# Performance work log

Hardware: AMD Instinct MI355X
Metric: run time of the kernel (lower is better)

## Reference

```python
import jax, jax.numpy as jnp
import numpy as np

# --- constants from the source module's globals ---
TAU_M, TAU_S = 8.0, 2.0
EM = float(np.exp(-1.0 / TAU_M))   # exp(-1/tau_m)
ES = float(np.exp(-1.0 / TAU_S))   # exp(-1/tau_s)
ETA = TAU_M / (TAU_M - TAU_S)
# dual-exponential PSP kernel eta*(e^{-t/tau_m}-e^{-t/tau_s}) as a 2nd-order IIR
A1_0 = EM + ES          # y[t-1] coefficient
A2_0 = -(EM * ES)       # y[t-2] coefficient
B_0 = ETA * (EM - ES)   # x[t] coefficient
THRESH, RESET_DECAY, RESET_V = 1.0, EM, 1.0
BATCH, T, IN = 64, 300, 300


def spike_fn(v):
    return (v >= THRESH).astype(v.dtype)


def dual_exp_iir(x, a1, a2, b):
    """Per-feature 2nd-order IIR over time. x: [B, F, T] -> [B, F, T]."""
    xt = jnp.moveaxis(x, -1, 0)  # [T, B, F]

    def step(carry, xc):
        y1, y2 = carry
        y = a1 * y1 + a2 * y2 + b * xc
        return (y, y1), y

    z = jnp.zeros_like(xt[0])
    _, ys = jax.lax.scan(step, (z, z), xt)
    return jnp.moveaxis(ys, 0, -1)


def lif_dense(x, W, bias):
    """Dense synapse + spiking neuron with decaying reset (membrane_filter=False).
    x: [B, Fin, T] -> spikes [B, Fout, T]."""
    # time-independent linear map: batch all T GEMMs into one einsum
    cur = jnp.einsum('bit,oi->bot', x, W) + bias[None, :, None]
    ct = jnp.moveaxis(cur, -1, 0)  # [T, B, Fout]

    def step(reset, c):
        v = c + reset                       # no membrane integration (membrane_filter=False)
        s = spike_fn(v)
        reset = reset * RESET_DECAY - s * RESET_V  # decaying post-spike reset
        return reset, s

    _, spikes = jax.lax.scan(step, jnp.zeros_like(ct[0]), ct)
    return jnp.moveaxis(spikes, 0, -1)


def setup_inputs() -> dict:
    key = jax.random.key(0)
    ks = jax.random.split(key, 8)
    inputs = (jax.random.uniform(ks[0], (BATCH, IN, T)) < 0.2).astype(jnp.float32)

    def coeffs(f):
        return (jnp.full((f,), A1_0, jnp.float32),
                jnp.full((f,), A2_0, jnp.float32),
                jnp.full((f,), B_0, jnp.float32))

    def dense(k, fin, fout):
        w = (jax.random.normal(k, (fout, fin), jnp.float32) / np.sqrt(fin)).astype(jnp.float32)
        return w, jnp.zeros((fout,), jnp.float32)

    a1_1, a2_1, b_1 = coeffs(300); W1, bias1 = dense(ks[1], 300, 500)
    a1_2, a2_2, b_2 = coeffs(500); W2, bias2 = dense(ks[2], 500, 200)
    a1_3, a2_3, b_3 = coeffs(200); W3, bias3 = dense(ks[3], 200, 500)
    a1_4, a2_4, b_4 = coeffs(500); W4, bias4 = dense(ks[4], 500, 300)
    return dict(inputs=inputs,
                a1_1=a1_1, a2_1=a2_1, b_1=b_1, W1=W1, bias1=bias1,
                a1_2=a1_2, a2_2=a2_2, b_2=b_2, W2=W2, bias2=bias2,
                a1_3=a1_3, a2_3=a2_3, b_3=b_3, W3=W3, bias3=bias3,
                a1_4=a1_4, a2_4=a2_4, b_4=b_4, W4=W4, bias4=bias4)


def reference(inputs, a1_1, a2_1, b_1, W1, bias1,
              a1_2, a2_2, b_2, W2, bias2,
              a1_3, a2_3, b_3, W3, bias3,
              a1_4, a2_4, b_4, W4, bias4):
    x = dual_exp_iir(inputs, a1_1, a2_1, b_1)
    s1 = lif_dense(x, W1, bias1)
    x = dual_exp_iir(s1, a1_2, a2_2, b_2)
    s2 = lif_dense(x, W2, bias2)
    x = dual_exp_iir(s2, a1_3, a2_3, b_3)
    s3 = lif_dense(x, W3, bias3)
    x = dual_exp_iir(s3, a1_4, a2_4, b_4)
    s4 = lif_dense(x, W4, bias4)
    # output filter: fixed (non-trainable) dual-exp IIR on the output spikes
    filt = dual_exp_iir(s4,
                        jnp.full((300,), A1_0, s4.dtype),
                        jnp.full((300,), A2_0, s4.dtype),
                        jnp.full((300,), B_0, s4.dtype))
    return (s4, filt)
```

## Files before the change

kernel.cpp:

```cpp
#include <hip/hip_runtime.h>

#define EMD 0.8824969025845955
#define ESD 0.6065306597126334
#define A1C ((float)(EMD + ESD))
#define A2C ((float)(-(EMD * ESD)))
#define BC  ((float)((8.0 / 6.0) * (EMD - ESD)))
#define EMF ((float)EMD)


__global__ __launch_bounds__(256) void prep_all(
    const float* __restrict__ W1, float* __restrict__ D1,
    const float* __restrict__ W2, float* __restrict__ D2,
    const float* __restrict__ W3, float* __restrict__ D3,
    const float* __restrict__ W4, float* __restrict__ D4,
    const float* __restrict__ inp, unsigned* __restrict__ M)
{
    __shared__ float tile[32][33];
    const int z  = blockIdx.z;
    const int tx = threadIdx.x;
    const int ty = threadIdx.y;
    const int c0 = blockIdx.x * 32;
    const int r0 = blockIdx.y * 32;

    if (z < 4) {
        int R, C; const float* S; float* D;
        switch (z) {
            case 0:  S = W1; D = D1; R = 500; C = 300; break;
            case 1:  S = W2; D = D2; R = 200; C = 500; break;
            case 2:  S = W3; D = D3; R = 500; C = 200; break;
            default: S = W4; D = D4; R = 300; C = 500; break;
        }
        if (c0 >= C || r0 >= R) return;
#pragma unroll
        for (int s = 0; s < 4; s++) {
            const int r = r0 + ty + 8 * s;
            const int c = c0 + tx;
            if (r < R && c < C) tile[ty + 8 * s][tx] = S[(size_t)r * C + c];
        }
        __syncthreads();
#pragma unroll
        for (int s = 0; s < 4; s++) {
            const int c = c0 + ty + 8 * s;
            const int r = r0 + tx;
            if (c < C && r < R) D[(size_t)c * R + r] = tile[tx][ty + 8 * s];
        }
        return;
    }

    if (c0 >= 300 || r0 >= 300) return;
    const int b = z - 4;
    const float* S = inp + (size_t)b * 90000;
#pragma unroll
    for (int s = 0; s < 4; s++) {
        const int r = r0 + ty + 8 * s;
        const int c = c0 + tx;
        tile[ty + 8 * s][tx] = (r < 300 && c < 300) ? S[(size_t)r * 300 + c] : 0.0f;
    }
    __syncthreads();
    const int wv   = ty >> 1;
    const int half = ty & 1;
#pragma unroll
    for (int s = 0; s < 4; s++) {
        const int tl = wv * 8 + s * 2 + half;
        const float v = tile[tx][tl];
        const unsigned long long mb = __ballot(v != 0.0f);
        const int t = c0 + tl;
        if (tx == 0 && t < 300) {
            const unsigned w32 = half ? (unsigned)(mb >> 32) : (unsigned)mb;
            M[((size_t)b * 300 + t) * 10 + (r0 >> 5)] = w32;
        }
    }
}

template<int OPL> struct VecSel;
template<> struct VecSel<2> { using T = float2; };
template<> struct VecSel<4> { using T = float4; };

__device__ __forceinline__ void vzero(float2& a){ a.x=0.f; a.y=0.f; }
__device__ __forceinline__ void vzero(float4& a){ a.x=0.f; a.y=0.f; a.z=0.f; a.w=0.f; }
__device__ __forceinline__ void vaccum(float2& a, const float2 w){ a.x+=w.x; a.y+=w.y; }
__device__ __forceinline__ void vaccum(float4& a, const float4 w){ a.x+=w.x; a.y+=w.y; a.z+=w.z; a.w+=w.w; }

#define WALK32(mw, accu, wl)                                                  \
    {                                                                         \
        unsigned mask_ = (mw);                                                \
        int n_ = __popc(mask_);                                               \
        while (n_ >= 4) {                                                     \
            const int j0_ = __builtin_ctz(mask_); mask_ &= mask_ - 1u;        \
            const int j1_ = __builtin_ctz(mask_); mask_ &= mask_ - 1u;        \
            const int j2_ = __builtin_ctz(mask_); mask_ &= mask_ - 1u;        \
            const int j3_ = __builtin_ctz(mask_); mask_ &= mask_ - 1u;        \
            const VT w0_ = *(const VT*)(&(wl)[j0_ * OCN]);                    \
            const VT w1_ = *(const VT*)(&(wl)[j1_ * OCN]);                    \
            const VT w2_ = *(const VT*)(&(wl)[j2_ * OCN]);                    \
            const VT w3_ = *(const VT*)(&(wl)[j3_ * OCN]);                    \
            vaccum(accu, w0_); vaccum(accu, w1_);                             \
            vaccum(accu, w2_); vaccum(accu, w3_);                             \
            n_ -= 4;                                                          \
        }                                                                     \
        if (n_ >= 2) {                                                        \
            const int j0_ = __builtin_ctz(mask_); mask_ &= mask_ - 1u;        \
            const int j1_ = __builtin_ctz(mask_); mask_ &= mask_ - 1u;        \
            const VT w0_ = *(const VT*)(&(wl)[j0_ * OCN]);                    \
            const VT w1_ = *(const VT*)(&(wl)[j1_ * OCN]);                    \
            vaccum(accu, w0_); vaccum(accu, w1_);                             \
            n_ -= 2;                                                          \
        }                                                                     \
        if (n_ > 0) {                                                         \
            const int j0_ = __builtin_ctz(mask_);                             \
            const VT w0_ = *(const VT*)(&(wl)[j0_ * OCN]);                    \
            vaccum(accu, w0_);                                                \
        }                                                                     \
    }

template<int OPL, int NU>
__global__ __launch_bounds__(256) void spmm_snn(
    const unsigned* __restrict__ M, const float* __restrict__ Wt,
    float* __restrict__ C, int K, int O, int T, int MW)
{
    constexpr int OCN = OPL * 64;
    constexpr int KG  = 32;
    constexpr int C4  = OCN / 4;
    constexpr int NF4 = KG * OCN / 1024;
    using VT = typename VecSel<OPL>::T;
    __shared__ float Wls[KG * OCN];
    const int tid  = threadIdx.x;
    const int lane = tid & 63;
    const int wv   = tid >> 6;
    const int oc   = blockIdx.x * OCN;
    const int t0   = blockIdx.y * (NU * 4);
    const int b    = blockIdx.z;

    const unsigned* Mb = M + (size_t)b * T * MW;
    float* Cb = C + (size_t)b * T * O;

    VT acc[NU];
#pragma unroll
    for (int u = 0; u < NU; u++) vzero(acc[u]);

    const int nkc = (K + KG - 1) / KG;
    float4 wpf[NF4];

#define LOADW(kc)                                                              \
    {                                                                          \
        const int kb_ = (kc) * KG;                                             \
        _Pragma("unroll")                                                      \
        for (int r = 0; r < NF4; r++) {                                        \
            const int idx = r * 256 + tid;                                     \
            const int k = kb_ + idx / C4;                                      \
            const int o = oc + (idx % C4) * 4;                                 \
            float4 w = make_float4(0.f, 0.f, 0.f, 0.f);                        \
            if (k < K && o + 3 < O)                                            \
                w = *reinterpret_cast<const float4*>(&Wt[(size_t)k * O + o]);  \
            wpf[r] = w;                                                        \
        }                                                                      \
    }

#define STOREW()                                                               \
    {                                                                          \
        _Pragma("unroll")                                                      \
        for (int r = 0; r < NF4; r++) {                                        \
            const int idx = r * 256 + tid;                                     \
            *reinterpret_cast<float4*>(                                        \
                &Wls[(idx / C4) * OCN + (idx % C4) * 4]) = wpf[r];             \
        }                                                                      \
    }

    const unsigned* mrow[NU];
    bool tvalid[NU];
#pragma unroll
    for (int u = 0; u < NU; u++) {
        const int t = t0 + u * 4 + wv;
        tvalid[u] = (t < T);
        mrow[u] = Mb + (size_t)(tvalid[u] ? t : 0) * MW;
    }

    unsigned mk[NU], mkn[NU];
#define LOADM(kc, dst)                                                         \
    {                                                                          \
        _Pragma("unroll")                                                      \
        for (int u = 0; u < NU; u++)                                           \
            dst[u] = tvalid[u] ? mrow[u][(kc)] : 0u;                           \
    }

    LOADW(0)
    LOADM(0, mk)
    STOREW()
    __syncthreads();

    const float* wl = &Wls[lane * OPL];

    for (int kc = 0; kc < nkc; kc++) {
        if (kc + 1 < nkc) {
            LOADW(kc + 1)
            LOADM(kc + 1, mkn)
        }

#pragma unroll
        for (int u = 0; u < NU; u++) {
            const unsigned m_ = (unsigned)__builtin_amdgcn_readfirstlane(mk[u]);
            WALK32(m_, acc[u], wl)
        }

        if (kc + 1 < nkc) {
            __syncthreads();
            STOREW()
#pragma unroll
            for (int u = 0; u < NU; u++) mk[u] = mkn[u];
            __syncthreads();
        }
    }

#pragma unroll
    for (int u = 0; u < NU; u++) {
        const int t = t0 + u * 4 + wv;
        const int o = oc + lane * OPL;
        if (t < T && o + OPL - 1 < O)
            *reinterpret_cast<VT*>(&Cb[(size_t)t * O + o]) = acc[u];
    }
#undef LOADW
#undef STOREW
#undef LOADM
}

#define LIF_STEP_S(xval, sval)                                                 \
    {                                                                          \
        const float y = A1 * y1 + A2 * y2 + Bc * (xval); y2 = y1; y1 = y;      \
        const float v = y + bi + r;                                            \
        sval = (v >= 1.0f) ? 1.0f : 0.0f;                                      \
        r = r * EMF - sval;                                                    \
    }

__global__ __launch_bounds__(64) void lif_pack(
    const float* __restrict__ C, unsigned* __restrict__ M,
    const float* __restrict__ bias,
    const float* __restrict__ a1p, const float* __restrict__ a2p,
    const float* __restrict__ bp, int O, int MW)
{
    const int lane = threadIdx.x;
    const int o = blockIdx.x * 64 + lane;
    const int b = blockIdx.y;
    if (o >= O) return;
    const float A1 = a1p[0], A2 = a2p[0], Bc = bp[0];
    const float bi = bias[o];
    const float* col = C + (size_t)b * 300 * O + o;
    unsigned long long* Mp =
        (unsigned long long*)(M + (size_t)b * 300 * MW);
    const int pair = blockIdx.x;
    const int hw   = MW >> 1;

    float pf[16];
#pragma unroll
    for (int u = 0; u < 16; u++) pf[u] = col[(size_t)u * O];

    float y1 = 0.f, y2 = 0.f, r = 0.f;
    for (int blk = 0; blk < 18; blk++) {
#pragma unroll
        for (int u = 0; u < 16; u++) {
            const int t = blk * 16 + u;
            const float x = pf[u];
            if (t + 16 < 300) pf[u] = col[(size_t)(t + 16) * O];
            float s;
            LIF_STEP_S(x, s)
            const unsigned long long mb = __ballot(s != 0.0f);
            if (lane == 0) Mp[(size_t)t * hw + pair] = mb;
        }
    }
#pragma unroll
    for (int u = 0; u < 12; u++) {
        const float x = pf[u];
        float s;
        LIF_STEP_S(x, s)
        const unsigned long long mb = __ballot(s != 0.0f);
        if (lane == 0) Mp[(size_t)(288 + u) * hw + pair] = mb;
    }
}

__global__ __launch_bounds__(64) void lif4_t(
    const float* __restrict__ Cc, float* __restrict__ S4,
    float* __restrict__ F, const float* __restrict__ bias,
    const float* __restrict__ a1p, const float* __restrict__ a2p,
    const float* __restrict__ bp, int O)
{
    const int o = blockIdx.x * 64 + threadIdx.x;
    const int b = blockIdx.y;
    if (o >= O) return;
    const float A1 = a1p[0], A2 = a2p[0], Bc = bp[0];
    const float bi = bias[o];
    const float* col = Cc + (size_t)b * 300 * O + o;
    float* scol = S4 + (size_t)b * 300 * O + o;
    float* fcol = F  + (size_t)b * 300 * O + o;

    float pf[16];
#pragma unroll
    for (int u = 0; u < 16; u++) pf[u] = col[(size_t)u * O];

    float y1 = 0.f, y2 = 0.f, r = 0.f;
    float z1 = 0.f, z2 = 0.f;
    for (int blk = 0; blk < 18; blk++) {
#pragma unroll
        for (int u = 0; u < 16; u++) {
            const int t = blk * 16 + u;
            const float x = pf[u];
            if (t + 16 < 300) pf[u] = col[(size_t)(t + 16) * O];
            float s;
            LIF_STEP_S(x, s)
            const float z = A1C * z1 + A2C * z2 + BC * s; z2 = z1; z1 = z;
            scol[(size_t)t * O] = s;
            fcol[(size_t)t * O] = z;
        }
    }
#pragma unroll
    for (int u = 0; u < 12; u++) {
        const int t = 288 + u;
        const float x = pf[u];
        float s;
        LIF_STEP_S(x, s)
        const float z = A1C * z1 + A2C * z2 + BC * s; z2 = z1; z1 = z;
        scol[(size_t)t * O] = s;
        fcol[(size_t)t * O] = z;
    }
}

__global__ __launch_bounds__(256) void transpose_out2(
    const float* __restrict__ s4, const float* __restrict__ flt,
    float* __restrict__ o1, float* __restrict__ o2)
{
    __shared__ float tile[32][33];
    const int z   = blockIdx.z;
    const int b   = z & 63;
    const int job = z >> 6;
    const float* S = (job ? flt : s4) + (size_t)b * 90000;
    float* D = (job ? o2 : o1) + (size_t)b * 90000;
    const int c0 = blockIdx.x * 32;
    const int r0 = blockIdx.y * 32;
    const int tx = threadIdx.x;
    const int ty = threadIdx.y;
#pragma unroll
    for (int s = 0; s < 4; s++) {
        const int r = r0 + ty + 8 * s;
        const int c = c0 + tx;
        if (r < 300 && c < 300) tile[ty + 8 * s][tx] = S[(size_t)r * 300 + c];
    }
    __syncthreads();
#pragma unroll
    for (int s = 0; s < 4; s++) {
        const int c = c0 + ty + 8 * s;
        const int r = r0 + tx;
        if (c < 300 && r < 300) D[(size_t)c * 300 + r] = tile[tx][ty + 8 * s];
    }
}

extern "C" void kernel_launch(void* const* d_in, const int* in_sizes, int n_in,
                              void* d_out, int out_size, void* d_ws, size_t ws_size,
                              hipStream_t stream)
{
    const float* inputs = (const float*)d_in[0];
    const float* a1_1 = (const float*)d_in[1];
    const float* a2_1 = (const float*)d_in[2];
    const float* b_1  = (const float*)d_in[3];
    const float* W1   = (const float*)d_in[4];
    const float* bias1= (const float*)d_in[5];
    const float* a1_2 = (const float*)d_in[6];
    const float* a2_2 = (const float*)d_in[7];
    const float* b_2  = (const float*)d_in[8];
    const float* W2   = (const float*)d_in[9];
    const float* bias2= (const float*)d_in[10];
    const float* a1_3 = (const float*)d_in[11];
    const float* a2_3 = (const float*)d_in[12];
    const float* b_3  = (const float*)d_in[13];
    const float* W3   = (const float*)d_in[14];
    const float* bias3= (const float*)d_in[15];
    const float* a1_4 = (const float*)d_in[16];
    const float* a2_4 = (const float*)d_in[17];
    const float* b_4  = (const float*)d_in[18];
    const float* W4   = (const float*)d_in[19];
    const float* bias4= (const float*)d_in[20];

    const int B = 64, T = 300;

    float* ws = (float*)d_ws;
    float* c1 = ws;
    float* c2 = ws + 9600000;
    float* spk4 = ws;
    float* flt4 = ws + 5760000;

    float* out = (float*)d_out;
    float* reg1 = out;
    float* reg2 = out + 5760000;
    float* Wt1 = reg1;
    float* Wt2 = reg1 + 150000;
    float* Wt3 = reg1 + 250000;
    float* Wt4 = reg1 + 350000;
    unsigned* m0 = (unsigned*)(reg1 + 500000);
    unsigned* m1 = (unsigned*)(reg1 + 692000);
    unsigned* m2 = (unsigned*)(reg1 + 999200);
    unsigned* m3 = (unsigned*)(reg1 + 1152800);

    const dim3 tb(32, 8);

    prep_all<<<dim3(16, 16, 68), tb, 0, stream>>>(W1, Wt1, W2, Wt2,
                                                  W3, Wt3, W4, Wt4,
                                                  inputs, m0);

    spmm_snn<4, 4><<<dim3(2, 19, B), 256, 0, stream>>>(m0, Wt1, c1, 300, 500, T, 10);
    lif_pack<<<dim3(8, B), 64, 0, stream>>>(c1, m1, bias1, a1_1, a2_1, b_1, 500, 16);
    spmm_snn<2, 8><<<dim3(2, 10, B), 256, 0, stream>>>(m1, Wt2, c2, 500, 200, T, 16);
    lif_pack<<<dim3(4, B), 64, 0, stream>>>(c2, m2, bias2, a1_2, a2_2, b_2, 200, 8);
    spmm_snn<4, 4><<<dim3(2, 19, B), 256, 0, stream>>>(m2, Wt3, c1, 200, 500, T, 8);
    lif_pack<<<dim3(8, B), 64, 0, stream>>>(c1, m3, bias3, a1_3, a2_3, b_3, 500, 16);
    spmm_snn<2, 8><<<dim3(3, 10, B), 256, 0, stream>>>(m3, Wt4, reg2, 500, 300, T, 16);
    lif4_t<<<dim3(5, B), 64, 0, stream>>>(reg2, spk4, flt4, bias4, a1_4, a2_4, b_4, 300);

    transpose_out2<<<dim3(10, 10, 128), tb, 0, stream>>>(spk4, flt4, reg1, reg2);
}
```

Baseline: 462.5 us.

## Store SpMM currents feature-major so LIF kernels read rows and drop transpose

The SpMM kernel now gives each wave a contiguous run of time steps and writes its output in [B, O, T] layout with float4 stores along time. The LIF and pack kernels then read each neuron's time series as contiguous float4 rows instead of strided columns. The final LIF kernel writes spikes and filtered outputs straight into the output buffers in the required layout, which removes the separate transpose kernel and its extra memory round trip. In exchange, the SpMM stores become scalar-per-feature strided writes across output rows, and the LIF threads now read widely separated rows, which can weaken coalescing.

```diff
diff --git a/kernel.cpp b/kernel.cpp
--- a/kernel.cpp
+++ b/kernel.cpp
@@ -80,6 +80,9 @@
 __device__ __forceinline__ void vzero(float4& a){ a.x=0.f; a.y=0.f; a.z=0.f; a.w=0.f; }
 __device__ __forceinline__ void vaccum(float2& a, const float2 w){ a.x+=w.x; a.y+=w.y; }
 __device__ __forceinline__ void vaccum(float4& a, const float4 w){ a.x+=w.x; a.y+=w.y; a.z+=w.z; a.w+=w.w; }
+__device__ __forceinline__ float vget(const float2& a, int j){ return j == 0 ? a.x : a.y; }
+__device__ __forceinline__ float vget(const float4& a, int j){
+    return j == 0 ? a.x : (j == 1 ? a.y : (j == 2 ? a.z : a.w)); }
 
 #define WALK32(mw, accu, wl)                                                  \
     {                                                                         \
@@ -130,9 +133,10 @@
     const int oc   = blockIdx.x * OCN;
     const int t0   = blockIdx.y * (NU * 4);
     const int b    = blockIdx.z;
+    const int twave = t0 + wv * NU;
 
     const unsigned* Mb = M + (size_t)b * T * MW;
-    float* Cb = C + (size_t)b * T * O;
+    float* Cb = C + (size_t)b * (size_t)O * T;
 
     VT acc[NU];
 #pragma unroll
@@ -170,7 +174,7 @@
     bool tvalid[NU];
 #pragma unroll
     for (int u = 0; u < NU; u++) {
-        const int t = t0 + u * 4 + wv;
+        const int t = twave + u;
         tvalid[u] = (t < T);
         mrow[u] = Mb + (size_t)(tvalid[u] ? t : 0) * MW;
     }
@@ -212,11 +216,23 @@
     }
 
 #pragma unroll
-    for (int u = 0; u < NU; u++) {
-        const int t = t0 + u * 4 + wv;
-        const int o = oc + lane * OPL;
-        if (t < T && o + OPL - 1 < O)
-            *reinterpret_cast<VT*>(&Cb[(size_t)t * O + o]) = acc[u];
+    for (int j = 0; j < OPL; j++) {
+        const int o = oc + lane * OPL + j;
+        if (o < O) {
+            float* orow = Cb + (size_t)o * T;
+#pragma unroll
+            for (int q = 0; q < NU / 4; q++) {
+                const int tq = twave + q * 4;
+                if (tq < T) {
+                    float4 v;
+                    v.x = vget(acc[q * 4 + 0], j);
+                    v.y = vget(acc[q * 4 + 1], j);
+                    v.z = vget(acc[q * 4 + 2], j);
+                    v.w = vget(acc[q * 4 + 3], j);
+                    *reinterpret_cast<float4*>(orow + tq) = v;
+                }
+            }
+        }
     }
 #undef LOADW
 #undef STOREW
@@ -230,6 +246,8 @@
         sval = (v >= 1.0f) ? 1.0f : 0.0f;                                      \
         r = r * EMF - sval;                                                    \
     }
+
+#define F4E(v, e) ((e) == 0 ? (v).x : (e) == 1 ? (v).y : (e) == 2 ? (v).z : (v).w)
 
 __global__ __launch_bounds__(64) void lif_pack(
     const float* __restrict__ C, unsigned* __restrict__ M,
@@ -243,36 +261,46 @@
     if (o >= O) return;
     const float A1 = a1p[0], A2 = a2p[0], Bc = bp[0];
     const float bi = bias[o];
-    const float* col = C + (size_t)b * 300 * O + o;
+    const float4* r4 = (const float4*)(C + ((size_t)b * O + o) * 300);
     unsigned long long* Mp =
         (unsigned long long*)(M + (size_t)b * 300 * MW);
     const int pair = blockIdx.x;
     const int hw   = MW >> 1;
 
-    float pf[16];
-#pragma unroll
-    for (int u = 0; u < 16; u++) pf[u] = col[(size_t)u * O];
+    float4 pf[4];
+#pragma unroll
+    for (int i = 0; i < 4; i++) pf[i] = r4[i];
 
     float y1 = 0.f, y2 = 0.f, r = 0.f;
     for (int blk = 0; blk < 18; blk++) {
 #pragma unroll
-        for (int u = 0; u < 16; u++) {
-            const int t = blk * 16 + u;
-            const float x = pf[u];
-            if (t + 16 < 300) pf[u] = col[(size_t)(t + 16) * O];
+        for (int q = 0; q < 4; q++) {
+            const float4 cur = pf[q];
+            const int nt = blk * 16 + q * 4 + 16;
+            if (nt < 300) pf[q] = r4[nt >> 2];
+#pragma unroll
+            for (int e = 0; e < 4; e++) {
+                const int t = blk * 16 + q * 4 + e;
+                const float x = F4E(cur, e);
+                float s;
+                LIF_STEP_S(x, s)
+                const unsigned long long mb = __ballot(s != 0.0f);
+                if (lane == 0) Mp[(size_t)t * hw + pair] = mb;
+            }
+        }
+    }
+#pragma unroll
+    for (int q = 0; q < 3; q++) {
+        const float4 cur = pf[q];
+#pragma unroll
+        for (int e = 0; e < 4; e++) {
+            const int t = 288 + q * 4 + e;
+            const float x = F4E(cur, e);
             float s;
             LIF_STEP_S(x, s)
             const unsigned long long mb = __ballot(s != 0.0f);
             if (lane == 0) Mp[(size_t)t * hw + pair] = mb;
         }
-    }
-#pragma unroll
-    for (int u = 0; u < 12; u++) {
-        const float x = pf[u];
-        float s;
-        LIF_STEP_S(x, s)
-        const unsigned long long mb = __ballot(s != 0.0f);
-        if (lane == 0) Mp[(size_t)(288 + u) * hw + pair] = mb;
     }
 }
 
@@ -287,67 +315,51 @@
     if (o >= O) return;
     const float A1 = a1p[0], A2 = a2p[0], Bc = bp[0];
     const float bi = bias[o];
-    const float* col = Cc + (size_t)b * 300 * O + o;
-    float* scol = S4 + (size_t)b * 300 * O + o;
-    float* fcol = F  + (size_t)b * 300 * O + o;
-
-    float pf[16];
-#pragma unroll
-    for (int u = 0; u < 16; u++) pf[u] = col[(size_t)u * O];
+    const float4* r4 = (const float4*)(Cc + ((size_t)b * O + o) * 300);
+    float4* s4r = (float4*)(S4 + ((size_t)b * O + o) * 300);
+    float4* f4r = (float4*)(F  + ((size_t)b * O + o) * 300);
+
+    float4 pf[4];
+#pragma unroll
+    for (int i = 0; i < 4; i++) pf[i] = r4[i];
 
     float y1 = 0.f, y2 = 0.f, r = 0.f;
     float z1 = 0.f, z2 = 0.f;
     for (int blk = 0; blk < 18; blk++) {
 #pragma unroll
-        for (int u = 0; u < 16; u++) {
-            const int t = blk * 16 + u;
-            const float x = pf[u];
-            if (t + 16 < 300) pf[u] = col[(size_t)(t + 16) * O];
+        for (int q = 0; q < 4; q++) {
+            const float4 cur = pf[q];
+            const int nt = blk * 16 + q * 4 + 16;
+            if (nt < 300) pf[q] = r4[nt >> 2];
+            float sv[4], zv[4];
+#pragma unroll
+            for (int e = 0; e < 4; e++) {
+                const float x = F4E(cur, e);
+                float s;
+                LIF_STEP_S(x, s)
+                const float z = A1C * z1 + A2C * z2 + BC * s; z2 = z1; z1 = z;
+                sv[e] = s; zv[e] = z;
+            }
+            const int fi = (blk * 16 + q * 4) >> 2;
+            s4r[fi] = make_float4(sv[0], sv[1], sv[2], sv[3]);
+            f4r[fi] = make_float4(zv[0], zv[1], zv[2], zv[3]);
+        }
+    }
+#pragma unroll
+    for (int q = 0; q < 3; q++) {
+        const float4 cur = pf[q];
+        float sv[4], zv[4];
+#pragma unroll
+        for (int e = 0; e < 4; e++) {
+            const float x = F4E(cur, e);
             float s;
             LIF_STEP_S(x, s)
             const float z = A1C * z1 + A2C * z2 + BC * s; z2 = z1; z1 = z;
-            scol[(size_t)t * O] = s;
-            fcol[(size_t)t * O] = z;
-        }
-    }
-#pragma unroll
-    for (int u = 0; u < 12; u++) {
-        const int t = 288 + u;
-        const float x = pf[u];
-        float s;
-        LIF_STEP_S(x, s)
-        const float z = A1C * z1 + A2C * z2 + BC * s; z2 = z1; z1 = z;
-        scol[(size_t)t * O] = s;
-        fcol[(size_t)t * O] = z;
-    }
-}
-
-__global__ __launch_bounds__(256) void transpose_out2(
-    const float* __restrict__ s4, const float* __restrict__ flt,
-    float* __restrict__ o1, float* __restrict__ o2)
-{
-    __shared__ float tile[32][33];
-    const int z   = blockIdx.z;
-    const int b   = z & 63;
-    const int job = z >> 6;
-    const float* S = (job ? flt : s4) + (size_t)b * 90000;
-    float* D = (job ? o2 : o1) + (size_t)b * 90000;
-    const int c0 = blockIdx.x * 32;
-    const int r0 = blockIdx.y * 32;
-    const int tx = threadIdx.x;
-    const int ty = threadIdx.y;
-#pragma unroll
-    for (int s = 0; s < 4; s++) {
-        const int r = r0 + ty + 8 * s;
-        const int c = c0 + tx;
-        if (r < 300 && c < 300) tile[ty + 8 * s][tx] = S[(size_t)r * 300 + c];
-    }
-    __syncthreads();
-#pragma unroll
-    for (int s = 0; s < 4; s++) {
-        const int c = c0 + ty + 8 * s;
-        const int r = r0 + tx;
-        if (c < 300 && r < 300) D[(size_t)c * 300 + r] = tile[tx][ty + 8 * s];
+            sv[e] = s; zv[e] = z;
+        }
+        const int fi = (288 + q * 4) >> 2;
+        s4r[fi] = make_float4(sv[0], sv[1], sv[2], sv[3]);
+        f4r[fi] = make_float4(zv[0], zv[1], zv[2], zv[3]);
     }
 }
 
@@ -382,8 +394,6 @@
     float* ws = (float*)d_ws;
     float* c1 = ws;
     float* c2 = ws + 9600000;
-    float* spk4 = ws;
-    float* flt4 = ws + 5760000;
 
     float* out = (float*)d_out;
     float* reg1 = out;
@@ -409,8 +419,6 @@
     lif_pack<<<dim3(4, B), 64, 0, stream>>>(c2, m2, bias2, a1_2, a2_2, b_2, 200, 8);
     spmm_snn<4, 4><<<dim3(2, 19, B), 256, 0, stream>>>(m2, Wt3, c1, 200, 500, T, 8);
     lif_pack<<<dim3(8, B), 64, 0, stream>>>(c1, m3, bias3, a1_3, a2_3, b_3, 500, 16);
-    spmm_snn<2, 8><<<dim3(3, 10, B), 256, 0, stream>>>(m3, Wt4, reg2, 500, 300, T, 16);
-    lif4_t<<<dim3(5, B), 64, 0, stream>>>(reg2, spk4, flt4, bias4, a1_4, a2_4, b_4, 300);
-
-    transpose_out2<<<dim3(10, 10, 128), tb, 0, stream>>>(spk4, flt4, reg1, reg2);
+    spmm_snn<2, 8><<<dim3(3, 10, B), 256, 0, stream>>>(m3, Wt4, c1, 500, 300, T, 16);
+    lif4_t<<<dim3(5, B), 64, 0, stream>>>(c1, reg1, reg2, bias4, a1_4, a2_4, b_4, 300);
 }
```

Result: faster. 385.0 us, median of 2 (-16.8%).
